# Kernel optimization log

Measured on AMD Instinct MI355X. Metric: run time of the kernel, lower is better.

Reference implementation:

```python
import jax, jax.numpy as jnp
import numpy as np

EPS = 1e-5


def setup_inputs() -> dict:
    key = jax.random.key(0)
    ks = jax.random.split(key, 12)
    B, C, H, W = 32, 512, 32, 32
    Ci = C // 2
    s_in = 1.0 / np.sqrt(C)
    s_ci = 1.0 / np.sqrt(Ci)
    return {
        "x": jax.random.normal(ks[0], (B, C, H, W), jnp.float32),
        # 1x1 conv weights stored as [out, in]
        "Wg": jax.random.normal(ks[1], (Ci, C), jnp.float32) * s_in,
        "bg": jax.random.normal(ks[2], (Ci,), jnp.float32) * 0.01,
        "Wt": jax.random.normal(ks[3], (Ci, C), jnp.float32) * s_in,
        "bt": jax.random.normal(ks[4], (Ci,), jnp.float32) * 0.01,
        "Wp": jax.random.normal(ks[5], (Ci, C), jnp.float32) * s_in,
        "bp": jax.random.normal(ks[6], (Ci,), jnp.float32) * 0.01,
        "Wz": jax.random.normal(ks[7], (C, Ci), jnp.float32) * s_ci,
        "bz": jax.random.normal(ks[8], (C,), jnp.float32) * 0.01,
        # BN affine params (torch inits these to 0 but we use nonzero for a meaningful baseline)
        "gamma": jax.random.normal(ks[9], (C,), jnp.float32) * 0.1,
        "beta": jax.random.normal(ks[10], (C,), jnp.float32) * 0.1,
    }


def reference(x, Wg, bg, Wt, bt, Wp, bp, Wz, bz, gamma, beta):
    B, C, H, W = x.shape
    N = H * W
    xr = x.reshape(B, C, N)
    # 1x1 conv projections (pure channel GEMMs)
    g_x = jnp.einsum('oc,bcn->bno', Wg, xr) + bg            # [B,N,Ci]
    theta_x = jnp.einsum('oc,bcn->bno', Wt, xr) + bt        # [B,N,Ci]
    phi_x = jnp.einsum('oc,bcn->bon', Wp, xr) + bp[None, :, None]  # [B,Ci,N]
    # full non-local attention over all N=H*W positions
    f = jnp.einsum('bnc,bcm->bnm', theta_x, phi_x)          # [B,N,N]
    attn = jax.nn.softmax(f, axis=-1)
    y = jnp.einsum('bnm,bmo->bon', attn, g_x)               # [B,Ci,N]
    # output 1x1 conv
    w_y = jnp.einsum('oc,bcn->bon', Wz, y) + bz[None, :, None]  # [B,C,N]
    # BatchNorm2d (training mode: batch statistics over B and spatial dims)
    mean = jnp.mean(w_y, axis=(0, 2), keepdims=True)
    var = jnp.var(w_y, axis=(0, 2), keepdims=True)
    w_y = (w_y - mean) / jnp.sqrt(var + EPS)
    w_y = w_y * gamma[None, :, None] + beta[None, :, None]
    return w_y.reshape(B, C, H, W) + x
```

## Files before the change

### kernel.cpp

```cpp
#include <hip/hip_runtime.h>
#include <math.h>

typedef __bf16 bf16;
typedef __bf16 bf16x8 __attribute__((ext_vector_type(8)));
typedef float f32x4 __attribute__((ext_vector_type(4)));
typedef unsigned short u16;
typedef unsigned int u32;

constexpr int BATCH = 32;
constexpr int CH    = 512;
constexpr int CI    = 256;
constexpr int NSP   = 1024;
constexpr int OCH   = 768;
constexpr float EPSV = 1e-5f;

__device__ __forceinline__ void gload_lds16(const bf16* g, bf16* l) {
    __builtin_amdgcn_global_load_lds(
        (const __attribute__((address_space(1))) void*)g,
        (__attribute__((address_space(3))) void*)l, 16, 0, 0);
}

__global__ void prep_weights(const float* __restrict__ Wg, const float* __restrict__ Wt,
                             const float* __restrict__ Wp, const float* __restrict__ Wz,
                             bf16* __restrict__ wc, bf16* __restrict__ wz,
                             float* __restrict__ sums) {
    int tid = blockIdx.x * 256 + threadIdx.x;
    if (tid < 1024) sums[tid] = 0.0f;
    if (tid < OCH * CH) {
        int r = tid / CH, c = tid % CH;
        float v;
        if (r < 256)      v = Wt[r * CH + c];
        else if (r < 512) v = Wp[(r - 256) * CH + c];
        else              v = Wg[(r - 512) * CH + c];
        wc[(size_t)(c >> 6) * (OCH * 64) + r * 64 + (c & 63)] = (bf16)v;
    } else {
        int t2 = tid - OCH * CH;
        if (t2 < CH * CI) {
            int r = t2 / CI, o = t2 % CI;
            wz[(size_t)(o >> 6) * (CH * 64) + r * 64 + (o & 63)] = (bf16)Wz[r * CI + o];
        }
    }
}

__global__ void transpose_x(const float* __restrict__ x, bf16* __restrict__ xb) {
    __shared__ bf16 tile[64][64];
    int b = blockIdx.z, kt = blockIdx.y, nb = blockIdx.x;
    int t = threadIdx.x;
    {
        int c_loc = t >> 2;
        int nq = t & 3;
        const float* src = x + ((size_t)b * CH + kt * 64 + c_loc) * NSP + nb * 64 + nq * 16;
        float vv[16];
        *(float4*)(vv + 0)  = *(const float4*)(src + 0);
        *(float4*)(vv + 4)  = *(const float4*)(src + 4);
        *(float4*)(vv + 8)  = *(const float4*)(src + 8);
        *(float4*)(vv + 12) = *(const float4*)(src + 12);
        int nbase = nq * 16;
        #pragma unroll
        for (int i = 0; i < 16; ++i) tile[nbase + i][c_loc] = (bf16)vv[i];
    }
    __syncthreads();
    {
        int n_loc = t >> 2;
        int cq = t & 3;
        bf16* dst = xb + ((((size_t)b * 8 + kt) * NSP) + nb * 64 + n_loc) * 64 + cq * 16;
        *(uint4*)(dst)     = *(const uint4*)&tile[n_loc][cq * 16];
        *(uint4*)(dst + 8) = *(const uint4*)&tile[n_loc][cq * 16 + 8];
    }
}

__launch_bounds__(256, 2)
__global__ void proj_gemm(const bf16* __restrict__ xb, const bf16* __restrict__ wc,
                          const float* __restrict__ bt, const float* __restrict__ bp,
                          const float* __restrict__ bg,
                          bf16* __restrict__ theta, bf16* __restrict__ phi_t,
                          bf16* __restrict__ gt_t) {
    constexpr int LDA = 72;
    __shared__ __align__(16) bf16 sm[2 * 128 * LDA];
    bf16* As = sm;
    bf16* Bs = sm + 128 * LDA;
    int b = blockIdx.z;
    int n0 = blockIdx.y * 128;
    int oc0 = blockIdx.x * 128;
    int t = threadIdx.x, lane = t & 63, wid = t >> 6;
    int wm = wid >> 1, wn = wid & 1;
    int l15 = lane & 15, quad = lane >> 4;

    f32x4 acc[4][4] = {};
    for (int kt = 0; kt < 8; ++kt) {
        __syncthreads();
        const bf16* asrc = xb + ((((size_t)b * 8 + kt) * NSP) + n0) * 64;
        const bf16* bsrc = wc + ((size_t)kt * OCH + oc0) * 64;
        for (int s = t; s < 1024; s += 256) {
            int row = s >> 3, c8 = s & 7;
            *(uint4*)&As[row * LDA + c8 * 8] = *(const uint4*)(asrc + (size_t)s * 8);
            *(uint4*)&Bs[row * LDA + c8 * 8] = *(const uint4*)(bsrc + (size_t)s * 8);
        }
        __syncthreads();
        #pragma unroll
        for (int kc = 0; kc < 2; ++kc) {
            bf16x8 af[4], bfv[4];
            #pragma unroll
            for (int i = 0; i < 4; ++i) {
                af[i]  = *(const bf16x8*)&As[(wm * 64 + i * 16 + l15) * LDA + kc * 32 + quad * 8];
                bfv[i] = *(const bf16x8*)&Bs[(wn * 64 + i * 16 + l15) * LDA + kc * 32 + quad * 8];
            }
            #pragma unroll
            for (int i = 0; i < 4; ++i)
                #pragma unroll
                for (int j = 0; j < 4; ++j)
                    acc[i][j] = __builtin_amdgcn_mfma_f32_16x16x32_bf16(af[i], bfv[j], acc[i][j], 0, 0, 0);
        }
    }
    if (oc0 < 256) {
        #pragma unroll
        for (int j = 0; j < 4; ++j) {
            int och = oc0 + wn * 64 + j * 16 + l15;
            float bv = bt[och];
            #pragma unroll
            for (int i = 0; i < 4; ++i) {
                int nrow = n0 + wm * 64 + i * 16 + quad * 4;
                bf16* p = theta + ((size_t)b * NSP + nrow) * CI + och;
                #pragma unroll
                for (int r = 0; r < 4; ++r)
                    p[(size_t)r * CI] = (bf16)(acc[i][j][r] + bv);
            }
        }
    } else if (oc0 < 512) {
        bf16* dstb = phi_t + (size_t)b * 262144;
        #pragma unroll
        for (int j = 0; j < 4; ++j) {
            int och = (oc0 - 256) + wn * 64 + j * 16 + l15;
            float bv = bp[och];
            int kc = och >> 5, qd = (och >> 3) & 3, e = och & 7;
            #pragma unroll
            for (int i = 0; i < 4; ++i) {
                int nrow = n0 + wm * 64 + i * 16 + quad * 4;
                int kt = nrow >> 5, h = (nrow >> 4) & 1;
                bf16* p = dstb + (size_t)kt * 8192 +
                          (size_t)(((h * 8 + kc) * 64 + qd * 16 + quad * 4) * 8) + e;
                #pragma unroll
                for (int r = 0; r < 4; ++r)
                    p[r * 8] = (bf16)(acc[i][j][r] + bv);
            }
        }
    } else {
        constexpr int LT = 136;
        int obase = oc0 - 512;
        __syncthreads();
        bf16* T = sm;
        #pragma unroll
        for (int j = 0; j < 4; ++j) {
            int och = wn * 64 + j * 16 + l15;
            float bv = bg[obase + och];
            #pragma unroll
            for (int i = 0; i < 4; ++i) {
                int nl = wm * 64 + i * 16 + quad * 4;
                bf16 tmp[4];
                #pragma unroll
                for (int r = 0; r < 4; ++r) tmp[r] = (bf16)(acc[i][j][r] + bv);
                *(uint2*)&T[och * LT + nl] = *(const uint2*)tmp;
            }
        }
        __syncthreads();
        bf16* dstb = gt_t + (size_t)b * 262144;
        for (int s = t; s < 2048; s += 256) {
            int row = s >> 4, part = s & 15;
            int o = obase + row;
            int kglob = n0 + part * 8;
            int kt = kglob >> 5, qd = (kglob >> 3) & 3;
            *(uint4*)(dstb + (size_t)kt * 8192 +
                      (size_t)(((o >> 4) * 64 + qd * 16 + (o & 15)) * 8)) =
                *(const uint4*)&T[row * LT + part * 8];
        }
    }
}

__launch_bounds__(256, 3)
__global__ void attn_kernel(const bf16* __restrict__ theta, const bf16* __restrict__ phi_t,
                            const bf16* __restrict__ gt_t, bf16* __restrict__ y) {
    constexpr int LP = 40;
    __shared__ __align__(16) char smem[54272];
    bf16* Ks = (bf16*)smem;
    bf16* Pw = (bf16*)(smem + 49152);

    int id = blockIdx.x;
    int j = id >> 3;
    int qt = j & 15;
    int b = (id & 7) + 8 * (j >> 4);

    int t = threadIdx.x, lane = t & 63, w = t >> 6;
    int l15 = lane & 15, quad = lane >> 4;

    const bf16* ph_b = phi_t + (size_t)b * 262144;
    const bf16* gt_b = gt_t + (size_t)b * 262144;

    bf16x8 qf[8];
    {
        const bf16* qrow = theta + ((size_t)b * NSP + qt * 64 + w * 16 + l15) * CI;
        #pragma unroll
        for (int kc = 0; kc < 8; ++kc)
            qf[kc] = *(const bf16x8*)(qrow + kc * 32 + quad * 8);
    }

    {
        const bf16* ksrc = ph_b + w * 2048 + lane * 8;
        const bf16* vsrc = gt_b + w * 2048 + lane * 8;
        bf16* kdst = Ks + w * 2048;
        bf16* vdst = (bf16*)(smem + 16384) + w * 2048;
        #pragma unroll
        for (int i = 0; i < 4; ++i) {
            gload_lds16(ksrc + i * 512, kdst + i * 512);
            gload_lds16(vsrc + i * 512, vdst + i * 512);
        }
    }
    __syncthreads();

    f32x4 oacc[16] = {};
    float m[4] = {-1e30f, -1e30f, -1e30f, -1e30f};
    float ps[4] = {0.f, 0.f, 0.f, 0.f};

    for (int kt = 0; kt < 32; ++kt) {
        bf16* Vc = (bf16*)(smem + 16384 + ((kt & 1) << 14));
        f32x4 s0 = {}, s1 = {};
        #pragma unroll
        for (int kc = 0; kc < 8; ++kc) {
            bf16x8 kf0 = *(const bf16x8*)(Ks + kc * 512 + lane * 8);
            bf16x8 kf1 = *(const bf16x8*)(Ks + 4096 + kc * 512 + lane * 8);
            s0 = __builtin_amdgcn_mfma_f32_16x16x32_bf16(qf[kc], kf0, s0, 0, 0, 0);
            s1 = __builtin_amdgcn_mfma_f32_16x16x32_bf16(qf[kc], kf1, s1, 0, 0, 0);
        }
        __syncthreads();
        if (kt < 31) {
            const bf16* ksrc = ph_b + (size_t)(kt + 1) * 8192 + w * 2048 + lane * 8;
            const bf16* vsrc = gt_b + (size_t)(kt + 1) * 8192 + w * 2048 + lane * 8;
            bf16* kdst = Ks + w * 2048;
            bf16* vdst = (bf16*)(smem + 16384 + (((kt + 1) & 1) << 14)) + w * 2048;
            #pragma unroll
            for (int i = 0; i < 4; ++i) {
                gload_lds16(ksrc + i * 512, kdst + i * 512);
                gload_lds16(vsrc + i * 512, vdst + i * 512);
            }
        }
        float cmx[4]; int flag = 0;
        #pragma unroll
        for (int r = 0; r < 4; ++r) {
            float c = fmaxf(s0[r], s1[r]);
            c = fmaxf(c, __shfl_xor(c, 1));
            c = fmaxf(c, __shfl_xor(c, 2));
            c = fmaxf(c, __shfl_xor(c, 4));
            c = fmaxf(c, __shfl_xor(c, 8));
            cmx[r] = c;
            flag |= (c > m[r]) ? 1 : 0;
        }
        if (__any(flag)) {
            float alpha[4];
            #pragma unroll
            for (int r = 0; r < 4; ++r) {
                float mn = fmaxf(m[r], cmx[r]);
                alpha[r] = __expf(m[r] - mn);
                m[r] = mn;
                ps[r] *= alpha[r];
            }
            #pragma unroll
            for (int nt = 0; nt < 16; ++nt) {
                oacc[nt][0] *= alpha[0];
                oacc[nt][1] *= alpha[1];
                oacc[nt][2] *= alpha[2];
                oacc[nt][3] *= alpha[3];
            }
        }
        #pragma unroll
        for (int r = 0; r < 4; ++r) {
            float p0 = __expf(s0[r] - m[r]);
            float p1 = __expf(s1[r] - m[r]);
            ps[r] += p0 + p1;
            Pw[(w * 16 + quad * 4 + r) * LP + l15]      = (bf16)p0;
            Pw[(w * 16 + quad * 4 + r) * LP + 16 + l15] = (bf16)p1;
        }
        bf16x8 pf = *(const bf16x8*)&Pw[(w * 16 + l15) * LP + quad * 8];
        #pragma unroll
        for (int nt = 0; nt < 16; ++nt) {
            bf16x8 vf = *(const bf16x8*)(Vc + nt * 512 + lane * 8);
            oacc[nt] = __builtin_amdgcn_mfma_f32_16x16x32_bf16(pf, vf, oacc[nt], 0, 0, 0);
        }
        __syncthreads();
    }

    #pragma unroll
    for (int r = 0; r < 4; ++r) {
        ps[r] += __shfl_xor(ps[r], 1);
        ps[r] += __shfl_xor(ps[r], 2);
        ps[r] += __shfl_xor(ps[r], 4);
        ps[r] += __shfl_xor(ps[r], 8);
    }
    float inv[4];
    #pragma unroll
    for (int r = 0; r < 4; ++r) inv[r] = 1.0f / ps[r];

    int nrow = qt * 64 + w * 16 + quad * 4;
    #pragma unroll
    for (int nt = 0; nt < 16; ++nt) {
        int o = nt * 16 + l15;
        bf16* dst = y + ((((size_t)b * 4 + (o >> 6)) * NSP) + nrow) * 64 + (o & 63);
        #pragma unroll
        for (int r = 0; r < 4; ++r)
            dst[(size_t)r * 64] = (bf16)(oacc[nt][r] * inv[r]);
    }
}

__launch_bounds__(256, 4)
__global__ void out_gemm(const bf16* __restrict__ y, const bf16* __restrict__ wz,
                         const float* __restrict__ bz, float* __restrict__ wy,
                         float* __restrict__ sums) {
    constexpr int LDA = 72;
    __shared__ __align__(16) bf16 As[128 * LDA];
    __shared__ __align__(16) bf16 Bs[128 * LDA];
    __shared__ float redS[128][2], redS2[128][2];
    int b = blockIdx.z;
    int co0 = blockIdx.y * 128;
    int n0 = blockIdx.x * 128;
    int t = threadIdx.x, lane = t & 63, wid = t >> 6;
    int wm = wid >> 1, wn = wid & 1;
    int l15 = lane & 15, quad = lane >> 4;

    f32x4 acc[4][4] = {};
    for (int kt = 0; kt < 4; ++kt) {
        __syncthreads();
        const bf16* asrc = wz + ((size_t)kt * CH + co0) * 64;
        const bf16* bsrc = y + ((((size_t)b * 4 + kt) * NSP) + n0) * 64;
        for (int s = t; s < 1024; s += 256) {
            int row = s >> 3, c8 = s & 7;
            *(uint4*)&As[row * LDA + c8 * 8] = *(const uint4*)(asrc + (size_t)s * 8);
            *(uint4*)&Bs[row * LDA + c8 * 8] = *(const uint4*)(bsrc + (size_t)s * 8);
        }
        __syncthreads();
        #pragma unroll
        for (int kc = 0; kc < 2; ++kc) {
            bf16x8 af[4], bfv[4];
            #pragma unroll
            for (int i = 0; i < 4; ++i) {
                af[i]  = *(const bf16x8*)&As[(wm * 64 + i * 16 + l15) * LDA + kc * 32 + quad * 8];
                bfv[i] = *(const bf16x8*)&Bs[(wn * 64 + i * 16 + l15) * LDA + kc * 32 + quad * 8];
            }
            #pragma unroll
            for (int i = 0; i < 4; ++i)
                #pragma unroll
                for (int j = 0; j < 4; ++j)
                    acc[i][j] = __builtin_amdgcn_mfma_f32_16x16x32_bf16(af[i], bfv[j], acc[i][j], 0, 0, 0);
        }
    }
    #pragma unroll
    for (int i = 0; i < 4; ++i) {
        int cbase = co0 + wm * 64 + i * 16 + quad * 4;
        #pragma unroll
        for (int r = 0; r < 4; ++r) {
            int c = cbase + r;
            float bv = bz[c];
            float s = 0.f, s2 = 0.f;
            #pragma unroll
            for (int jj = 0; jj < 4; ++jj) {
                int n = n0 + wn * 64 + jj * 16 + l15;
                float v = acc[i][jj][r] + bv;
                wy[((size_t)b * CH + c) * NSP + n] = v;
                s += v; s2 += v * v;
            }
            s  += __shfl_xor(s, 1);  s2 += __shfl_xor(s2, 1);
            s  += __shfl_xor(s, 2);  s2 += __shfl_xor(s2, 2);
            s  += __shfl_xor(s, 4);  s2 += __shfl_xor(s2, 4);
            s  += __shfl_xor(s, 8);  s2 += __shfl_xor(s2, 8);
            if (l15 == 0) {
                int cl = wm * 64 + i * 16 + quad * 4 + r;
                redS[cl][wn]  = s;
                redS2[cl][wn] = s2;
            }
        }
    }
    __syncthreads();
    if (t < 128) {
        atomicAdd(&sums[co0 + t],      redS[t][0] + redS[t][1]);
        atomicAdd(&sums[CH + co0 + t], redS2[t][0] + redS2[t][1]);
    }
}

__global__ void bn_finalize(float* __restrict__ out, const float* __restrict__ x,
                            const float* __restrict__ sums,
                            const float* __restrict__ gamma, const float* __restrict__ beta) {
    size_t idx4 = (size_t)blockIdx.x * 256 + threadIdx.x;
    size_t flat = idx4 * 4;
    int ch = (int)((flat >> 10) & 511);
    float S = sums[ch], S2 = sums[CH + ch];
    const float invcnt = 1.0f / (BATCH * NSP);
    float mean = S * invcnt;
    float var = S2 * invcnt - mean * mean;
    float sc = rsqrtf(var + EPSV) * gamma[ch];
    float bi = beta[ch] - mean * sc;
    float4 wv = *(float4*)(out + flat);
    float4 xv = *(const float4*)(x + flat);
    wv.x = wv.x * sc + bi + xv.x;
    wv.y = wv.y * sc + bi + xv.y;
    wv.z = wv.z * sc + bi + xv.z;
    wv.w = wv.w * sc + bi + xv.w;
    *(float4*)(out + flat) = wv;
}

extern "C" void kernel_launch(void* const* d_in, const int* in_sizes, int n_in,
                              void* d_out, int out_size, void* d_ws, size_t ws_size,
                              hipStream_t stream) {
    const float* x     = (const float*)d_in[0];
    const float* Wg    = (const float*)d_in[1];
    const float* bg    = (const float*)d_in[2];
    const float* Wt    = (const float*)d_in[3];
    const float* bt    = (const float*)d_in[4];
    const float* Wp    = (const float*)d_in[5];
    const float* bp    = (const float*)d_in[6];
    const float* Wz    = (const float*)d_in[7];
    const float* bz    = (const float*)d_in[8];
    const float* gamma = (const float*)d_in[9];
    const float* beta  = (const float*)d_in[10];
    float* out = (float*)d_out;

    char* ws = (char*)d_ws;
    bf16*  y_t   = (bf16*)(ws);
    bf16*  g_t   = (bf16*)(ws + 16777216);
    bf16*  wc    = (bf16*)(ws + 33554432);
    bf16*  wzb   = (bf16*)(ws + 34340864);
    float* sums  = (float*)(ws + 34603008);

    char* ob = (char*)d_out;
    bf16* xb    = (bf16*)(ob);
    bf16* theta = (bf16*)(ob + 33554432);
    bf16* phi_t = (bf16*)(ob + 50331648);

    prep_weights<<<dim3(2048), dim3(256), 0, stream>>>(Wg, Wt, Wp, Wz, wc, wzb, sums);
    transpose_x<<<dim3(16, 8, 32), dim3(256), 0, stream>>>(x, xb);
    proj_gemm<<<dim3(6, 8, 32), dim3(256), 0, stream>>>(xb, wc, bt, bp, bg, theta, phi_t, g_t);
    attn_kernel<<<dim3(512), dim3(256), 0, stream>>>(theta, phi_t, g_t, y_t);
    out_gemm<<<dim3(8, 4, 32), dim3(256), 0, stream>>>(y_t, wzb, bz, out, sums);
    bn_finalize<<<dim3(16384), dim3(256), 0, stream>>>(out, x, sums, gamma, beta);
}
```

Baseline: 310.9 us.

## Double-buffer K tiles, prefetch before compute, lazy softmax rescale, raise MFMA priority

K tiles are now double-buffered like V, so the next K/V tile load is issued at the start of each iteration. This removes the mid-iteration __syncthreads that previously guarded the single K buffer. The online-softmax rescale now fires only when the row max grows by more than 8, which cuts rescale work but lets exponentials reach up to e^8 before correction. s_setprio is raised around the MFMA loops. LDS grows to about 69KB and launch bounds drop from 3 to 2 blocks per CU, reducing occupancy.

Measured after the change: 299.7 us. -3.6%, faster.

```diff
diff --git a/kernel.cpp b/kernel.cpp
--- a/kernel.cpp
+++ b/kernel.cpp
@@ -176,13 +176,12 @@
     }
 }
 
-__launch_bounds__(256, 3)
+__launch_bounds__(256, 2)
 __global__ void attn_kernel(const bf16* __restrict__ theta, const bf16* __restrict__ phi_t,
                             const bf16* __restrict__ gt_t, bf16* __restrict__ y) {
     constexpr int LP = 40;
-    __shared__ __align__(16) char smem[54272];
-    bf16* Ks = (bf16*)smem;
-    bf16* Pw = (bf16*)(smem + 49152);
+    __shared__ __align__(16) char smem[70656];
+    bf16* Pw = (bf16*)(smem + 65536);
 
     int id = blockIdx.x;
     int j = id >> 3;
@@ -192,8 +191,8 @@
     int t = threadIdx.x, lane = t & 63, w = t >> 6;
     int l15 = lane & 15, quad = lane >> 4;
 
-    const bf16* ph_b = phi_t + (size_t)b * 262144;
-    const bf16* gt_b = gt_t + (size_t)b * 262144;
+    const bf16* ph_b = phi_t + (size_t)b * 262144 + w * 2048 + lane * 8;
+    const bf16* gt_b = gt_t + (size_t)b * 262144 + w * 2048 + lane * 8;
 
     bf16x8 qf[8];
     {
@@ -204,14 +203,12 @@
     }
 
     {
-        const bf16* ksrc = ph_b + w * 2048 + lane * 8;
-        const bf16* vsrc = gt_b + w * 2048 + lane * 8;
-        bf16* kdst = Ks + w * 2048;
-        bf16* vdst = (bf16*)(smem + 16384) + w * 2048;
+        bf16* kdst = (bf16*)(smem)         + w * 2048;
+        bf16* vdst = (bf16*)(smem + 32768) + w * 2048;
         #pragma unroll
         for (int i = 0; i < 4; ++i) {
-            gload_lds16(ksrc + i * 512, kdst + i * 512);
-            gload_lds16(vsrc + i * 512, vdst + i * 512);
+            gload_lds16(ph_b + i * 512, kdst + i * 512);
+            gload_lds16(gt_b + i * 512, vdst + i * 512);
         }
     }
     __syncthreads();
@@ -221,27 +218,33 @@
     float ps[4] = {0.f, 0.f, 0.f, 0.f};
 
     for (int kt = 0; kt < 32; ++kt) {
-        bf16* Vc = (bf16*)(smem + 16384 + ((kt & 1) << 14));
+        int cur = kt & 1;
+        bf16* Kc = (bf16*)(smem + (cur << 14));
+        bf16* Vc = (bf16*)(smem + 32768 + (cur << 14));
+
+        if (kt < 31) {
+            const bf16* ksrc = ph_b + (size_t)(kt + 1) * 8192;
+            const bf16* vsrc = gt_b + (size_t)(kt + 1) * 8192;
+            bf16* kdst = (bf16*)(smem + ((1 - cur) << 14)) + w * 2048;
+            bf16* vdst = (bf16*)(smem + 32768 + ((1 - cur) << 14)) + w * 2048;
+            #pragma unroll
+            for (int i = 0; i < 4; ++i) {
+                gload_lds16(ksrc + i * 512, kdst + i * 512);
+                gload_lds16(vsrc + i * 512, vdst + i * 512);
+            }
+        }
+
         f32x4 s0 = {}, s1 = {};
+        __builtin_amdgcn_s_setprio(1);
         #pragma unroll
         for (int kc = 0; kc < 8; ++kc) {
-            bf16x8 kf0 = *(const bf16x8*)(Ks + kc * 512 + lane * 8);
-            bf16x8 kf1 = *(const bf16x8*)(Ks + 4096 + kc * 512 + lane * 8);
+            bf16x8 kf0 = *(const bf16x8*)(Kc + kc * 512 + lane * 8);
+            bf16x8 kf1 = *(const bf16x8*)(Kc + 4096 + kc * 512 + lane * 8);
             s0 = __builtin_amdgcn_mfma_f32_16x16x32_bf16(qf[kc], kf0, s0, 0, 0, 0);
             s1 = __builtin_amdgcn_mfma_f32_16x16x32_bf16(qf[kc], kf1, s1, 0, 0, 0);
         }
-        __syncthreads();
-        if (kt < 31) {
-            const bf16* ksrc = ph_b + (size_t)(kt + 1) * 8192 + w * 2048 + lane * 8;
-            const bf16* vsrc = gt_b + (size_t)(kt + 1) * 8192 + w * 2048 + lane * 8;
-            bf16* kdst = Ks + w * 2048;
-            bf16* vdst = (bf16*)(smem + 16384 + (((kt + 1) & 1) << 14)) + w * 2048;
-            #pragma unroll
-            for (int i = 0; i < 4; ++i) {
-                gload_lds16(ksrc + i * 512, kdst + i * 512);
-                gload_lds16(vsrc + i * 512, vdst + i * 512);
-            }
-        }
+        __builtin_amdgcn_s_setprio(0);
+
         float cmx[4]; int flag = 0;
         #pragma unroll
         for (int r = 0; r < 4; ++r) {
@@ -251,7 +254,7 @@
             c = fmaxf(c, __shfl_xor(c, 4));
             c = fmaxf(c, __shfl_xor(c, 8));
             cmx[r] = c;
-            flag |= (c > m[r]) ? 1 : 0;
+            flag |= (c > m[r] + 8.0f) ? 1 : 0;
         }
         if (__any(flag)) {
             float alpha[4];
@@ -278,12 +281,16 @@
             Pw[(w * 16 + quad * 4 + r) * LP + l15]      = (bf16)p0;
             Pw[(w * 16 + quad * 4 + r) * LP + 16 + l15] = (bf16)p1;
         }
+
         bf16x8 pf = *(const bf16x8*)&Pw[(w * 16 + l15) * LP + quad * 8];
+        __builtin_amdgcn_s_setprio(1);
         #pragma unroll
         for (int nt = 0; nt < 16; ++nt) {
             bf16x8 vf = *(const bf16x8*)(Vc + nt * 512 + lane * 8);
             oacc[nt] = __builtin_amdgcn_mfma_f32_16x16x32_bf16(pf, vf, oacc[nt], 0, 0, 0);
         }
+        __builtin_amdgcn_s_setprio(0);
+
         __syncthreads();
     }
 
```
